# Kernel tuning notes

Measured on AMD Instinct MI355X. Metric: run time of the kernel, lower is better.

## Reference

```python
import jax, jax.numpy as jnp
import numpy as np

B, N, M, D = 2, 16384, 4096, 128  # batch, points, voxels, d_model (= d_points)


def _mlp(x, W1, b1, W2, b2):
    # Linear -> ReLU -> Linear (matches nn.Sequential(Linear, ReLU, Linear))
    return jax.nn.relu(x @ W1 + b1) @ W2 + b2


def setup_inputs() -> dict:
    key = jax.random.key(0)
    ks = jax.random.split(key, 12)
    s = 0.02
    inp = {
        "p_xyz": jax.random.normal(ks[0], (B, N, 3), jnp.float32),
        "v_xyz": jax.random.normal(ks[1], (B, 3), jnp.float32),
        "p_features": jax.random.normal(ks[2], (B, N, D), jnp.float32),
        "v_featrues": jax.random.normal(ks[3], (B, M, D), jnp.float32),
    }

    def two_layer(k, din):
        k1, k2 = jax.random.split(k)
        return (jax.random.normal(k1, (din, D), jnp.float32) * s,
                jnp.zeros((D,), jnp.float32),
                jax.random.normal(k2, (D, D), jnp.float32) * s,
                jnp.zeros((D,), jnp.float32))

    for name, din, k in (("alpha", D, ks[4]), ("beta", D, ks[5]),
                         ("omega", D, ks[6]), ("delta", 3, ks[7])):
        W1, b1, W2, b2 = two_layer(k, din)
        inp[name + "_W1"] = W1
        inp[name + "_b1"] = b1
        inp[name + "_W2"] = W2
        inp[name + "_b2"] = b2
    return inp


def reference(p_xyz, v_xyz, p_features, v_featrues,
              alpha_W1, alpha_b1, alpha_W2, alpha_b2,
              beta_W1, beta_b1, beta_W2, beta_b2,
              omega_W1, omega_b1, omega_W2, omega_b2,
              delta_W1, delta_b1, delta_W2, delta_b2):
    # dist = |p_xyz - v_xyz| per batch: [B, N, 3]
    dist = jnp.abs(p_xyz - v_xyz[:, None, :])
    pv = _mlp(dist, delta_W1, delta_b1, delta_W2, delta_b2)        # [B, N, D]
    q = _mlp(v_featrues, alpha_W1, alpha_b1, alpha_W2, alpha_b2)   # [B, M, D]
    k = _mlp(p_features, beta_W1, beta_b1, beta_W2, beta_b2)       # [B, N, D]
    v = _mlp(p_features, omega_W1, omega_b1, omega_W2, omega_b2)   # [B, N, D]
    # q@k^T + q@pv^T == q@(k+pv)^T : [B, M, N]
    scale = 1.0 / jnp.sqrt(jnp.asarray(D, dtype=q.dtype))
    scores = jnp.einsum('bmd,bnd->bmn', q, k + pv) * scale
    # softmax over dim=-2 (the query/voxel dim M), as in the original
    w = jax.nn.softmax(scores, axis=-2)                            # [B, M, N]
    res = jnp.einsum('bmn,bnd->bmd', w, v)                         # [B, M, D]
    return res + v_featrues
```

## Files before the change

kernel.cpp:

```cpp
#include <hip/hip_runtime.h>

#define B_ 2
#define N_ 16384
#define M_ 4096
#define D_ 128

typedef __attribute__((ext_vector_type(8))) short s8;
typedef __attribute__((ext_vector_type(4))) float f4;
typedef __attribute__((ext_vector_type(16))) float f16v;
typedef __attribute__((ext_vector_type(4))) unsigned short us4;
typedef unsigned short u16;

__device__ __forceinline__ u16 f2b(float f) {
  unsigned int x = __float_as_uint(f);
  unsigned int r = x + 0x7fffu + ((x >> 16) & 1u);
  return (u16)(r >> 16);
}
__device__ __forceinline__ s8 ld8(const u16* p) {
  return *reinterpret_cast<const s8*>(p);
}
__device__ __forceinline__ s8 ldcvt8(const float* p) {
  f4 x = *reinterpret_cast<const f4*>(p);
  f4 y = *reinterpret_cast<const f4*>(p + 4);
  s8 r;
  r[0] = (short)f2b(x[0]); r[1] = (short)f2b(x[1]);
  r[2] = (short)f2b(x[2]); r[3] = (short)f2b(x[3]);
  r[4] = (short)f2b(y[0]); r[5] = (short)f2b(y[1]);
  r[6] = (short)f2b(y[2]); r[7] = (short)f2b(y[3]);
  return r;
}
__device__ __forceinline__ f4 mfma16(s8 a, s8 b, f4 c) {
  return __builtin_amdgcn_mfma_f32_16x16x32_bf16(a, b, c, 0, 0, 0);
}
__device__ __forceinline__ f16v mfma32(s8 a, s8 b, f16v c) {
  return __builtin_amdgcn_mfma_f32_32x32x16_bf16(a, b, c, 0, 0, 0);
}
__device__ __forceinline__ int swz(int row, int off) {
  return (row << 8) + ((((off >> 4) ^ (row & 15)) << 4) | (off & 15));
}
#define CS 0.1275174365f

__device__ __forceinline__ void lds_barrier() {
  asm volatile("s_waitcnt lgkmcnt(0)" ::: "memory");
  __builtin_amdgcn_s_barrier();
}

__global__ __launch_bounds__(256) void wtrans(
    const float* a0, const float* a1, const float* a2, const float* a3,
    const float* a4, const float* a5, const float* a6, u16* dst) {
  const int mat = blockIdx.x >> 4, part = blockIdx.x & 15;
  const float* s;
  switch (mat) {
    case 0: s = a0; break; case 1: s = a1; break; case 2: s = a2; break;
    case 3: s = a3; break; case 4: s = a4; break; case 5: s = a5; break;
    default: s = a6; break;
  }
  u16* d = dst + mat * 16384 + part * 1024;
  const int o0 = part * 1024;
  for (int i = threadIdx.x; i < 1024; i += 256) {
    const int o = o0 + i;
    const int c = o >> 7, r = o & 127;
    d[i] = f2b(s[r * 128 + c]);
  }
}

__global__ __launch_bounds__(256) void mlps(
    const float* __restrict__ vfeat,
    const u16* __restrict__ aW1t, const float* __restrict__ ab1,
    const u16* __restrict__ aW2t, const float* __restrict__ ab2,
    u16* __restrict__ qbuf,
    const float* __restrict__ pf, const float* __restrict__ pxyz,
    const float* __restrict__ vxyz,
    const u16* __restrict__ bW1t, const float* __restrict__ bb1,
    const u16* __restrict__ bW2t, const float* __restrict__ bb2,
    const float* __restrict__ dW1, const float* __restrict__ db1,
    const u16* __restrict__ dW2t, const float* __restrict__ db2,
    const u16* __restrict__ oW1t, const float* __restrict__ ob1,
    const u16* __restrict__ oW2t, const float* __restrict__ ob2,
    u16* __restrict__ kpv_out, u16* __restrict__ vt_out) {
  __shared__ u16 H1[64][136];
  __shared__ u16 H2[64][136];
  __shared__ u16 H3[64][136];
  const int tid = threadIdx.x;
  const int wave = tid >> 6, lane = tid & 63;
  const int c16 = lane & 15, quad = lane >> 4;

  if (blockIdx.x < 256) {
    const int rowg = wave & 1, nsh = wave >> 1;
    const long row0 = (long)blockIdx.x * 32 + rowg * 16;
    s8 a[4];
    {
      const float* xr = vfeat + (row0 + c16) * D_ + quad * 8;
      #pragma unroll
      for (int kk = 0; kk < 4; kk++) a[kk] = ldcvt8(xr + kk * 32);
    }
    #pragma unroll
    for (int ns = 0; ns < 4; ns++) {
      f4 acc = {0.f, 0.f, 0.f, 0.f};
      const int c = (nsh * 4 + ns) * 16 + c16;
      const u16* wr = aW1t + (long)c * 128 + quad * 8;
      #pragma unroll
      for (int kk = 0; kk < 4; kk++) acc = mfma16(a[kk], ld8(wr + kk * 32), acc);
      const float bias = ab1[c];
      #pragma unroll
      for (int r = 0; r < 4; r++) {
        float v = acc[r] + bias;
        H1[rowg * 16 + quad * 4 + r][c] = f2b(v > 0.f ? v : 0.f);
      }
    }
    __syncthreads();
    s8 a2[4];
    #pragma unroll
    for (int kk = 0; kk < 4; kk++)
      a2[kk] = *reinterpret_cast<const s8*>(&H1[rowg * 16 + c16][kk * 32 + quad * 8]);
    #pragma unroll
    for (int ns = 0; ns < 4; ns++) {
      f4 acc = {0.f, 0.f, 0.f, 0.f};
      const int c = (nsh * 4 + ns) * 16 + c16;
      const u16* wr = aW2t + (long)c * 128 + quad * 8;
      #pragma unroll
      for (int kk = 0; kk < 4; kk++) acc = mfma16(a2[kk], ld8(wr + kk * 32), acc);
      const float bias = ab2[c];
      #pragma unroll
      for (int r = 0; r < 4; r++)
        qbuf[(row0 + quad * 4 + r) * D_ + c] = f2b(acc[r] + bias);
    }
    return;
  }
  const int bx = blockIdx.x - 256;
  const long row0 = (long)bx * 64 + wave * 16;
  s8 a[4];
  {
    const float* xr = pf + (row0 + c16) * D_ + quad * 8;
    #pragma unroll
    for (int kk = 0; kk < 4; kk++) a[kk] = ldcvt8(xr + kk * 32);
  }
  #pragma unroll
  for (int ns = 0; ns < 8; ns++) {
    f4 accb = {0.f, 0.f, 0.f, 0.f}, acco = {0.f, 0.f, 0.f, 0.f};
    const int c = ns * 16 + c16;
    const u16* wrb = bW1t + (long)c * 128 + quad * 8;
    const u16* wro = oW1t + (long)c * 128 + quad * 8;
    #pragma unroll
    for (int kk = 0; kk < 4; kk++) {
      accb = mfma16(a[kk], ld8(wrb + kk * 32), accb);
      acco = mfma16(a[kk], ld8(wro + kk * 32), acco);
    }
    const float biasb = bb1[c], biaso = ob1[c];
    #pragma unroll
    for (int r = 0; r < 4; r++) {
      float vb = accb[r] + biasb;
      float vo = acco[r] + biaso;
      H1[wave * 16 + quad * 4 + r][c] = f2b(vb > 0.f ? vb : 0.f);
      H3[wave * 16 + quad * 4 + r][c] = f2b(vo > 0.f ? vo : 0.f);
    }
  }
  {
    const long bat = ((long)bx * 64) / N_;
    const float vx0 = vxyz[bat * 3 + 0];
    const float vx1 = vxyz[bat * 3 + 1];
    const float vx2 = vxyz[bat * 3 + 2];
    for (int i = 0; i < 32; i++) {
      const int e = lane + 64 * i;
      const int rr = e >> 7, cc = e & 127;
      const long gr = row0 + rr;
      const float d0 = fabsf(pxyz[gr * 3 + 0] - vx0);
      const float d1 = fabsf(pxyz[gr * 3 + 1] - vx1);
      const float d2 = fabsf(pxyz[gr * 3 + 2] - vx2);
      float h = d0 * dW1[cc] + d1 * dW1[128 + cc] + d2 * dW1[256 + cc] + db1[cc];
      H2[wave * 16 + rr][cc] = f2b(h > 0.f ? h : 0.f);
    }
  }
  __syncthreads();
  s8 ab[4], ad[4], ao[4];
  #pragma unroll
  for (int kk = 0; kk < 4; kk++) {
    ab[kk] = *reinterpret_cast<const s8*>(&H1[wave * 16 + c16][kk * 32 + quad * 8]);
    ad[kk] = *reinterpret_cast<const s8*>(&H2[wave * 16 + c16][kk * 32 + quad * 8]);
    ao[kk] = *reinterpret_cast<const s8*>(&H3[wave * 16 + c16][kk * 32 + quad * 8]);
  }
  #pragma unroll
  for (int ns = 0; ns < 8; ns++) {
    const int c = ns * 16 + c16;
    f4 acck = {0.f, 0.f, 0.f, 0.f};
    f4 accv = {0.f, 0.f, 0.f, 0.f};
    const u16* wrb = bW2t + (long)c * 128 + quad * 8;
    const u16* wrd = dW2t + (long)c * 128 + quad * 8;
    const u16* wro = oW2t + (long)c * 128 + quad * 8;
    #pragma unroll
    for (int kk = 0; kk < 4; kk++) {
      acck = mfma16(ab[kk], ld8(wrb + kk * 32), acck);
      acck = mfma16(ad[kk], ld8(wrd + kk * 32), acck);
      accv = mfma16(ao[kk], ld8(wro + kk * 32), accv);
    }
    const float biask = bb2[c] + db2[c];
    const float biasv = ob2[c];
    #pragma unroll
    for (int r = 0; r < 4; r++)
      kpv_out[(row0 + quad * 4 + r) * D_ + c] = f2b(acck[r] + biask);
    {
      const long g = row0 + quad * 4;
      const long bb = g >> 14;
      const long n = g & (N_ - 1);
      us4 pk;
      #pragma unroll
      for (int r = 0; r < 4; r++) pk[r] = f2b(accv[r] + biasv);
      *reinterpret_cast<us4*>(vt_out + bb * (long)128 * N_ + (long)c * N_ + n) = pk;
    }
  }
}

__global__ __launch_bounds__(512, 6) void colsum_v2c(const u16* __restrict__ q,
    const u16* __restrict__ kpv, float* __restrict__ sums) {
  __shared__ char LQ[16384];
  const int tid = threadIdx.x;
  const int wave = tid >> 6, lane = tid & 63;
  const int c16 = lane & 15, quad = lane >> 4;
  const int mh = blockIdx.x & 3;
  const int nb = ((blockIdx.x >> 2) & 127) * 128 + wave * 16;
  const int b = blockIdx.x >> 9;
  const int rsub = lane >> 4, ch = lane & 15;

  s8 ak[4];
  {
    const u16* kr = kpv + ((long)b * N_ + nb + c16) * D_ + quad * 8;
    #pragma unroll
    for (int kk = 0; kk < 4; kk++) ak[kk] = ld8(kr + kk * 32);
  }
  f4 sum = {0.f, 0.f, 0.f, 0.f};
  const u16* qb = q + (long)b * M_ * D_ + (long)mh * (M_ / 4) * D_;

  for (int m0 = 0; m0 < M_ / 4; m0 += 64) {
    s8 t0 = ld8(qb + (long)(m0 + wave * 8 + rsub) * D_ + ch * 8);
    s8 t1 = ld8(qb + (long)(m0 + wave * 8 + 4 + rsub) * D_ + ch * 8);
    *reinterpret_cast<s8*>(LQ + swz(wave * 8 + rsub, ch * 16)) = t0;
    *reinterpret_cast<s8*>(LQ + swz(wave * 8 + 4 + rsub, ch * 16)) = t1;
    __syncthreads();
    #pragma unroll
    for (int ms = 0; ms < 4; ms++) {
      f4 st = {0.f, 0.f, 0.f, 0.f};
      #pragma unroll
      for (int kk = 0; kk < 4; kk++) {
        s8 bq = *reinterpret_cast<const s8*>(LQ + swz(ms * 16 + c16, kk * 64 + quad * 16));
        st = mfma16(ak[kk], bq, st);
      }
      #pragma unroll
      for (int r = 0; r < 4; r++) sum[r] += exp2f(st[r] * CS);
    }
    __syncthreads();
  }
  #pragma unroll
  for (int mask = 1; mask < 16; mask <<= 1) {
    #pragma unroll
    for (int r = 0; r < 4; r++) sum[r] += __shfl_xor(sum[r], mask, 64);
  }
  if (c16 == 0)
    *reinterpret_cast<f4*>(sums + (long)mh * (B_ * N_) + (long)b * N_ + nb + quad * 4) = sum;
}

__global__ __launch_bounds__(256) void recip_k(const float* __restrict__ sums,
                                               float* __restrict__ l2ic) {
  const int i = blockIdx.x * 256 + threadIdx.x;
  const float s = sums[i] + sums[B_ * N_ + i] + sums[2 * B_ * N_ + i]
                + sums[3 * B_ * N_ + i];
  l2ic[i] = -log2f(s);
}

__global__ __launch_bounds__(256, 2) void attn_v13(const u16* __restrict__ q,
    const u16* __restrict__ kpv, const u16* __restrict__ vt,
    const float* __restrict__ l2ic, float* __restrict__ part,
    int lgns, int nslice) {
  __shared__ char LK[16384];
  __shared__ char LP[16384];
  const int tid = threadIdx.x;
  const int wave = tid >> 6, lane = tid & 63;
  const int l31 = lane & 31, hi = lane >> 5;
  const int bid = blockIdx.x;
  const int ns = bid & ((1 << lgns) - 1);
  const int mb = (bid >> lgns) & 31;
  const int b = bid >> (lgns + 5);
  const int nt = wave & 1, mth = wave >> 1;
  const int m_base = mb * 128;
  const int n_begin = ns * nslice;
  const int rsub = lane >> 4, ch = lane & 15;

  const u16* kpb = kpv + (long)b * N_ * D_;
  const u16* vtb = vt + (long)b * (long)D_ * N_;
  const float* l2b = l2ic + (long)b * N_;

  s8 bq[2][8];
  #pragma unroll
  for (int t = 0; t < 2; t++) {
    const u16* qr = q + ((long)b * M_ + m_base + (mth + 2 * t) * 32 + l31) * D_ + hi * 8;
    #pragma unroll
    for (int kk = 0; kk < 8; kk++) bq[t][kk] = ld8(qr + kk * 16);
  }
  f16v acc[4];
  #pragma unroll
  for (int i = 0; i < 4; i++)
    #pragma unroll
    for (int r = 0; r < 16; r++) acc[i][r] = 0.f;

  s8 tmp[4];
  #pragma unroll
  for (int i = 0; i < 4; i++)
    tmp[i] = ld8(kpb + (long)(n_begin + wave * 16 + i * 4 + rsub) * D_ + ch * 8);

  for (int n0 = n_begin; n0 < n_begin + nslice; n0 += 64) {
    #pragma unroll
    for (int i = 0; i < 4; i++)
      *reinterpret_cast<s8*>(LK + swz(wave * 16 + i * 4 + rsub, ch * 16)) = tmp[i];
    {
      int nn = n0 + 64;
      if (nn >= n_begin + nslice) nn = n_begin;
      #pragma unroll
      for (int i = 0; i < 4; i++)
        tmp[i] = ld8(kpb + (long)(nn + wave * 16 + i * 4 + rsub) * D_ + ch * 8);
    }
    lds_barrier();
    s8 bv[4];
    #pragma unroll
    for (int kk = 0; kk < 4; kk++)
      bv[kk] = ld8(vtb + (long)(wave * 32 + l31) * N_ + n0 + kk * 16 + hi * 8);
    {
      f16v st0, st1;
      #pragma unroll
      for (int r = 0; r < 16; r++) { st0[r] = 0.f; st1[r] = 0.f; }
      #pragma unroll
      for (int kk = 0; kk < 8; kk++) {
        s8 aK = *reinterpret_cast<const s8*>(
            LK + swz(nt * 32 + l31, kk * 32 + hi * 16));
        st0 = mfma32(aK, bq[0][kk], st0);
        st1 = mfma32(aK, bq[1][kk], st1);
      }
      #pragma unroll
      for (int g = 0; g < 4; g++) {
        const f4 l2 = *reinterpret_cast<const f4*>(l2b + n0 + nt * 32 + 8 * g + 4 * hi);
        us4 pk0, pk1;
        #pragma unroll
        for (int r = 0; r < 4; r++) {
          pk0[r] = (u16)(__float_as_uint(exp2f(fmaf(st0[g * 4 + r], CS, l2[r]))) >> 16);
          pk1[r] = (u16)(__float_as_uint(exp2f(fmaf(st1[g * 4 + r], CS, l2[r]))) >> 16);
        }
        *reinterpret_cast<us4*>(LP + (4 * nt + g) * 2048
                                + ((mth + 0) * 32 + l31) * 16 + 8 * hi) = pk0;
        *reinterpret_cast<us4*>(LP + (4 * nt + g) * 2048
                                + ((mth + 2) * 32 + l31) * 16 + 8 * hi) = pk1;
      }
    }
    lds_barrier();
    #pragma unroll
    for (int kk = 0; kk < 4; kk++) {
      #pragma unroll
      for (int i = 0; i < 4; i++) {
        s8 ap = *reinterpret_cast<const s8*>(
            LP + (2 * kk + hi) * 2048 + (i * 32 + l31) * 16);
        acc[i] = mfma32(ap, bv[kk], acc[i]);
      }
    }
  }
  float* pt = part + (long)bid * 128 * 128;
  #pragma unroll
  for (int i = 0; i < 4; i++)
    #pragma unroll
    for (int g = 0; g < 4; g++)
      #pragma unroll
      for (int r = 0; r < 4; r++)
        pt[(i * 32 + g * 8 + 4 * hi + r) * 128 + wave * 32 + l31] = acc[i][g * 4 + r];
}

__global__ __launch_bounds__(256) void attn_reduce(const float* __restrict__ part,
    const float* __restrict__ vfeat, float* __restrict__ out, int nsplit) {
  const int g4 = blockIdx.x * 256 + threadIdx.x;
  const int b = g4 >> 17;
  const int rem = g4 & 131071;
  const int m = rem >> 5;
  const int d4 = rem & 31;
  const int mb = m >> 7, mr = m & 127;
  const long base = ((long)(b * 32 + mb) * nsplit) * 16384 + mr * 128 + d4 * 4;
  f4 s = *reinterpret_cast<const f4*>(vfeat + (long)g4 * 4);
  for (int ns = 0; ns < nsplit; ns++)
    s += *reinterpret_cast<const f4*>(part + base + ns * 16384);
  *reinterpret_cast<f4*>(out + (long)g4 * 4) = s;
}

extern "C" void kernel_launch(void* const* d_in, const int* in_sizes, int n_in,
                              void* d_out, int out_size, void* d_ws, size_t ws_size,
                              hipStream_t stream) {
  const float* p_xyz  = (const float*)d_in[0];
  const float* v_xyz  = (const float*)d_in[1];
  const float* p_feat = (const float*)d_in[2];
  const float* v_feat = (const float*)d_in[3];
  const float* aW1 = (const float*)d_in[4],  *ab1 = (const float*)d_in[5];
  const float* aW2 = (const float*)d_in[6],  *ab2 = (const float*)d_in[7];
  const float* bW1 = (const float*)d_in[8],  *bb1 = (const float*)d_in[9];
  const float* bW2 = (const float*)d_in[10], *bb2 = (const float*)d_in[11];
  const float* oW1 = (const float*)d_in[12], *ob1 = (const float*)d_in[13];
  const float* oW2 = (const float*)d_in[14], *ob2 = (const float*)d_in[15];
  const float* dW1 = (const float*)d_in[16], *db1 = (const float*)d_in[17];
  const float* dW2 = (const float*)d_in[18], *db2 = (const float*)d_in[19];

  char* ws = (char*)d_ws;
  u16* wt    = (u16*)ws;
  u16* aW1t  = wt + 0 * 16384;
  u16* aW2t  = wt + 1 * 16384;
  u16* bW1t  = wt + 2 * 16384;
  u16* bW2t  = wt + 3 * 16384;
  u16* oW1t  = wt + 4 * 16384;
  u16* oW2t  = wt + 5 * 16384;
  u16* dW2t  = wt + 6 * 16384;
  u16* qbuf  = (u16*)(ws + 262144);
  u16* kpvb  = (u16*)(ws + 2359296);
  u16* vtb   = (u16*)(ws + 10747904);
  float* invb = (float*)(ws + 19136512);
  float* partb = (float*)(ws + 19267584);
  float* sums  = partb;

  const size_t part_off = 19267584;
  int lgns = (ws_size >= part_off + (size_t)8 * B_ * M_ * D_ * 4) ? 3 : 2;
  const int nsplit = 1 << lgns;
  const int nslice = N_ / nsplit;

  wtrans<<<dim3(112), dim3(256), 0, stream>>>(aW1, aW2, bW1, bW2, oW1, oW2, dW2, wt);
  mlps<<<dim3(256 + (B_ * N_) / 64), dim3(256), 0, stream>>>(
      v_feat, aW1t, ab1, aW2t, ab2, qbuf,
      p_feat, p_xyz, v_xyz, bW1t, bb1, bW2t, bb2, dW1, db1, dW2t, db2,
      oW1t, ob1, oW2t, ob2, kpvb, vtb);
  colsum_v2c<<<dim3(B_ * 128 * 4), dim3(512), 0, stream>>>(qbuf, kpvb, sums);
  recip_k<<<dim3((B_ * N_) / 256), dim3(256), 0, stream>>>(sums, invb);
  attn_v13<<<dim3(B_ * 32 * nsplit), dim3(256), 0, stream>>>(qbuf, kpvb, vtb, invb,
                                                             partb, lgns, nslice);
  attn_reduce<<<dim3((B_ * M_ * D_ / 4) / 256), dim3(256), 0, stream>>>(partb, v_feat,
                                                                        (float*)d_out,
                                                                        nsplit);
}
```

Before: 289.5 us.

## Double-buffer Q tiles in column-sum kernel with register prefetch

The column-sum kernel now loads 128-row Q tiles into two alternating LDS buffers. The next tile is prefetched into registers while MFMAs run on the current one, and one barrier per step replaces two. This is meant to hide global-load latency and cut synchronisation overhead. In exchange, LDS use grows from 16KB to 64KB per block and the occupancy hint drops from 6 to 4.

```diff
diff --git a/kernel.cpp b/kernel.cpp
--- a/kernel.cpp
+++ b/kernel.cpp
@@ -210,9 +210,9 @@
   }
 }
 
-__global__ __launch_bounds__(512, 6) void colsum_v2c(const u16* __restrict__ q,
+__global__ __launch_bounds__(512, 4) void colsum_v3(const u16* __restrict__ q,
     const u16* __restrict__ kpv, float* __restrict__ sums) {
-  __shared__ char LQ[16384];
+  __shared__ char LQ[2][32768];
   const int tid = threadIdx.x;
   const int wave = tid >> 6, lane = tid & 63;
   const int c16 = lane & 15, quad = lane >> 4;
@@ -230,24 +230,40 @@
   f4 sum = {0.f, 0.f, 0.f, 0.f};
   const u16* qb = q + (long)b * M_ * D_ + (long)mh * (M_ / 4) * D_;
 
-  for (int m0 = 0; m0 < M_ / 4; m0 += 64) {
-    s8 t0 = ld8(qb + (long)(m0 + wave * 8 + rsub) * D_ + ch * 8);
-    s8 t1 = ld8(qb + (long)(m0 + wave * 8 + 4 + rsub) * D_ + ch * 8);
-    *reinterpret_cast<s8*>(LQ + swz(wave * 8 + rsub, ch * 16)) = t0;
-    *reinterpret_cast<s8*>(LQ + swz(wave * 8 + 4 + rsub, ch * 16)) = t1;
-    __syncthreads();
-    #pragma unroll
-    for (int ms = 0; ms < 4; ms++) {
+  s8 t[4];
+  #pragma unroll
+  for (int i = 0; i < 4; i++)
+    t[i] = ld8(qb + (long)(wave * 16 + i * 4 + rsub) * D_ + ch * 8);
+  #pragma unroll
+  for (int i = 0; i < 4; i++)
+    *reinterpret_cast<s8*>(LQ[0] + swz(wave * 16 + i * 4 + rsub, ch * 16)) = t[i];
+
+  for (int s = 0; s < 8; s++) {
+    lds_barrier();
+    const int m1 = (s + 1) * 128;
+    if (s < 7) {
+      #pragma unroll
+      for (int i = 0; i < 4; i++)
+        t[i] = ld8(qb + (long)(m1 + wave * 16 + i * 4 + rsub) * D_ + ch * 8);
+    }
+    const char* lq = LQ[s & 1];
+    #pragma unroll
+    for (int ms = 0; ms < 8; ms++) {
       f4 st = {0.f, 0.f, 0.f, 0.f};
       #pragma unroll
       for (int kk = 0; kk < 4; kk++) {
-        s8 bq = *reinterpret_cast<const s8*>(LQ + swz(ms * 16 + c16, kk * 64 + quad * 16));
+        s8 bq = *reinterpret_cast<const s8*>(lq + swz(ms * 16 + c16, kk * 64 + quad * 16));
         st = mfma16(ak[kk], bq, st);
       }
       #pragma unroll
       for (int r = 0; r < 4; r++) sum[r] += exp2f(st[r] * CS);
     }
-    __syncthreads();
+    if (s < 7) {
+      #pragma unroll
+      for (int i = 0; i < 4; i++)
+        *reinterpret_cast<s8*>(LQ[(s + 1) & 1]
+            + swz(wave * 16 + i * 4 + rsub, ch * 16)) = t[i];
+    }
   }
   #pragma unroll
   for (int mask = 1; mask < 16; mask <<= 1) {
@@ -426,7 +442,7 @@
       v_feat, aW1t, ab1, aW2t, ab2, qbuf,
       p_feat, p_xyz, v_xyz, bW1t, bb1, bW2t, bb2, dW1, db1, dW2t, db2,
       oW1t, ob1, oW2t, ob2, kpvb, vtb);
-  colsum_v2c<<<dim3(B_ * 128 * 4), dim3(512), 0, stream>>>(qbuf, kpvb, sums);
+  colsum_v3<<<dim3(B_ * 128 * 4), dim3(512), 0, stream>>>(qbuf, kpvb, sums);
   recip_k<<<dim3((B_ * N_) / 256), dim3(256), 0, stream>>>(sums, invb);
   attn_v13<<<dim3(B_ * 32 * nsplit), dim3(256), 0, stream>>>(qbuf, kpvb, vtb, invb,
                                                              partb, lgns, nslice);
```

Result: no change. 292.4 us (+1.0%).
